# Optimization experiments

Hardware: AMD Instinct MI355X
Metric: run time of the kernel (lower is better)

The kernel has to match this reference:

```python
import jax, jax.numpy as jnp
import numpy as np

K = 3  # dynamic kernel size


def _conv(x, w, b, pad):
    # x: [B,Cin,H,W], w: [Cout,Cin,kh,kw]
    y = jax.lax.conv_general_dilated(
        x, w, window_strides=(1, 1), padding=pad,
        dimension_numbers=("NCHW", "OIHW", "NCHW"))
    return y + b[None, :, None, None]


def setup_inputs() -> dict:
    key = jax.random.key(0)
    ks = jax.random.split(key, 9)
    B, C, H, W = 16, 256, 64, 64
    sc1 = 1.0 / np.sqrt(C * 9)
    sc3 = 1.0 / np.sqrt(C)
    return {
        "x":    jax.random.normal(ks[0], (B, C, H, W), jnp.float32),
        "kin":  jax.random.normal(ks[1], (B, C, H, W), jnp.float32),
        "w1":   jax.random.normal(ks[2], (C, C, 3, 3), jnp.float32) * sc1,
        "b1":   jax.random.normal(ks[3], (C,), jnp.float32) * 0.01,
        "w2":   jax.random.normal(ks[4], (C, C, 3, 3), jnp.float32) * sc1,
        "b2":   jax.random.normal(ks[5], (C,), jnp.float32) * 0.01,
        "w3":   jax.random.normal(ks[6], (K * K * C, C, 1, 1), jnp.float32) * sc3,
        "b3":   jax.random.normal(ks[7], (K * K * C,), jnp.float32) * 0.01,
        "bias": jax.random.normal(ks[8], (C,), jnp.float32) * 0.01,
    }


def reference(x, kin, w1, b1, w2, b2, w3, b3, bias):
    B, C, H, W = x.shape
    # tokernel: conv3x3 (valid) -> lrelu(0.1) -> conv3x3 -> lrelu -> global avg pool -> 1x1 conv
    h = jax.nn.leaky_relu(_conv(kin, w1, b1, "VALID"), 0.1)
    h = jax.nn.leaky_relu(_conv(h, w2, b2, "VALID"), 0.1)
    p = h.mean(axis=(2, 3))                                   # [B,C] adaptive avg pool 1x1
    kern = jnp.einsum("bc,oc->bo", p, w3.reshape(K * K * C, C)) + b3  # 1x1 conv
    kern = kern.reshape(B, C, 1, K, K)                        # per-sample depthwise weights

    pad = [(K // 2, K // 2)] * 2

    def dw(xi, wi):  # xi: [C,H,W], wi: [C,1,K,K]
        return jax.lax.conv_general_dilated(
            xi[None], wi, window_strides=(1, 1), padding=pad,
            dimension_numbers=("NCHW", "OIHW", "NCHW"),
            feature_group_count=C)[0]

    y = jax.vmap(dw)(x, kern)                                 # [B,C,H,W]
    return y + bias[None, :, None, None]
```

## Files before the change

kernel.cpp:

```cpp
#include <hip/hip_runtime.h>
#include <hip/hip_bf16.h>
#include <stdint.h>

#define CCH 256

typedef __attribute__((ext_vector_type(8))) short short8;
typedef __attribute__((ext_vector_type(4))) float f32x4;

__device__ __forceinline__ float lrelu(float v) { return v > 0.f ? v : 0.1f * v; }

__device__ __forceinline__ unsigned short f2bf(float f) {
    __hip_bfloat16 h = __float2bfloat16(f);
    return *reinterpret_cast<unsigned short*>(&h);
}

__device__ __forceinline__ void gl_lds16(const void* g, void* s) {
    __builtin_amdgcn_global_load_lds(
        (const __attribute__((address_space(1))) unsigned int*)(uintptr_t)g,
        (__attribute__((address_space(3))) unsigned int*)(unsigned int)(uintptr_t)s,
        16, 0, 0);
}

__device__ __forceinline__ void pipe_barrier() {
    asm volatile("" ::: "memory");
    __builtin_amdgcn_s_barrier();
    asm volatile("" ::: "memory");
}

__global__ __launch_bounds__(256)
void nhwc_k(const float* __restrict__ in, unsigned short* __restrict__ out)
{
    __shared__ float t[32][65];
    const int tid = threadIdx.x;
    const int kc = blockIdx.x, y = blockIdx.y, b = blockIdx.z;
    const float* src = in + ((size_t)(b * 256 + kc * 32)) * 4096 + y * 64;
#pragma unroll
    for (int i = 0; i < 2; ++i) {
        int idx = tid + i * 256;
        int cl = idx >> 4, xg = idx & 15;
        float4 v = *(const float4*)(src + (size_t)cl * 4096 + xg * 4);
        t[cl][xg * 4 + 0] = v.x; t[cl][xg * 4 + 1] = v.y;
        t[cl][xg * 4 + 2] = v.z; t[cl][xg * 4 + 3] = v.w;
    }
    __syncthreads();
    const int x = tid >> 2, cg = tid & 3;
    union { unsigned short us[8]; uint4 v; } u;
#pragma unroll
    for (int j = 0; j < 8; ++j) u.us[j] = f2bf(t[cg * 8 + j][x]);
    unsigned short* dst = out + (((size_t)(b * 8 + kc) * 4096 + y * 64 + x) * 32 + cg * 8);
    *(uint4*)dst = u.v;
}

__global__ __launch_bounds__(256)
void wtr_k(const float* __restrict__ w1, const float* __restrict__ w2,
           unsigned short* __restrict__ o1, unsigned short* __restrict__ o2)
{
    const int ss = blockIdx.x;
    const int kc = ss / 9, t = ss - kc * 9;
    const float* w = blockIdx.y ? w2 : w1;
    unsigned short* o = blockIdx.y ? o2 : o1;
#pragma unroll
    for (int rep = 0; rep < 4; ++rep) {
        int slot = threadIdx.x + rep * 256;
        int f = slot >> 6, l = slot & 63;
        int co = f * 16 + (l & 15);
        int q  = l >> 4;
        union { unsigned short us[8]; uint4 v; } u;
#pragma unroll
        for (int uu = 0; uu < 8; ++uu)
            u.us[uu] = f2bf(w[((size_t)co * 256 + kc * 32 + q * 8 + uu) * 9 + t]);
        *(uint4*)(o + (size_t)ss * 8192 + slot * 8) = u.v;
    }
}

__global__ __launch_bounds__(256)
void zero_pool_k(float* __restrict__ p) { p[blockIdx.x * 256 + threadIdx.x] = 0.f; }

template<int POOL, int WIN, int WOUT>
__global__ __launch_bounds__(256, 2)
void convmm_k(const unsigned short* __restrict__ im, const unsigned short* __restrict__ wt,
              const float* __restrict__ bias, unsigned short* __restrict__ outp,
              float* __restrict__ pool)
{
    constexpr int HINPIX = WIN * WIN;
    constexpr int NVAL   = WOUT * WOUT;
    constexpr int NB = 16 * 512 + 8 * 512;
    __shared__ __align__(16) short Ls[3 * NB];

    const int tid  = threadIdx.x;
    const int wave = tid >> 6;
    const int lane = tid & 63;
    const int quad = lane >> 4;
    const int l15  = lane & 15;
    const int wm   = (wave & 1) * 128;
    const int wn   = (wave >> 1) * 64;
    const int nb0  = blockIdx.x * 128;
    const int b    = blockIdx.y;

    const unsigned short* abase = wt + (size_t)(wave * 4) * 512 + (size_t)lane * 8;
    size_t bofs[2];
#pragma unroll
    for (int h = 0; h < 2; ++h) {
        int nn = nb0 + (wave * 2 + h) * 16 + l15;
        if (nn > NVAL - 1) nn = NVAL - 1;
        int y = nn / WOUT, x = nn - y * WOUT;
        bofs[h] = ((size_t)(b * 8) * HINPIX + (size_t)y * WIN + x) * 32 + quad * 8;
    }

    f32x4 acc[8][4];
#pragma unroll
    for (int i = 0; i < 8; ++i)
#pragma unroll
        for (int j = 0; j < 4; ++j) { f32x4 z = {0.f, 0.f, 0.f, 0.f}; acc[i][j] = z; }

    auto stage = [&](int ss, short* buf) {
        const int kc = ss / 9, t = ss - kc * 9;
        const int ky = t / 3, kx = t - ky * 3;
        const size_t aoff = (size_t)ss * 8192;
        const size_t boff = ((size_t)kc * HINPIX + (size_t)ky * WIN + kx) * 32;
        short* bl = buf + 16 * 512;
#pragma unroll
        for (int h = 0; h < 4; ++h)
            gl_lds16(abase + aoff + h * 512, buf + (wave * 4 + h) * 512);
#pragma unroll
        for (int h = 0; h < 2; ++h)
            gl_lds16(im + bofs[h] + boff, bl + (wave * 2 + h) * 512);
    };

    auto compute = [&](const short* buf) {
        const short* ap = buf + (size_t)(wave & 1) * 8 * 512 + lane * 8;
        const short* bp = buf + 16 * 512 + (size_t)(wave >> 1) * 4 * 512 + lane * 8;
        short8 a[8], bfr[4];
#pragma unroll
        for (int i = 0; i < 8; ++i)
            a[i]  = *(const short8*)(ap + i * 512);
#pragma unroll
        for (int j = 0; j < 4; ++j)
            bfr[j] = *(const short8*)(bp + j * 512);
        __builtin_amdgcn_s_setprio(1);
#pragma unroll
        for (int i = 0; i < 8; ++i)
#pragma unroll
            for (int j = 0; j < 4; ++j)
                acc[i][j] = __builtin_amdgcn_mfma_f32_16x16x32_bf16(a[i], bfr[j], acc[i][j], 0, 0, 0);
        __builtin_amdgcn_s_setprio(0);
    };

    short* B0 = Ls;
    short* B1 = Ls + NB;
    short* B2 = Ls + 2 * NB;

    stage(0, B0);
    stage(1, B1);
    asm volatile("s_waitcnt vmcnt(6)" ::: "memory");
    pipe_barrier();

    short *c0 = B0, *c1 = B1, *c2 = B2;
    for (int s = 0; s < 70; ++s) {
        stage(s + 2, c2);
        compute(c0);
        asm volatile("s_waitcnt vmcnt(6)" ::: "memory");
        pipe_barrier();
        short* t = c0; c0 = c1; c1 = c2; c2 = t;
    }
    compute(c0);
    asm volatile("s_waitcnt vmcnt(0)" ::: "memory");
    pipe_barrier();
    compute(c1);

    const int co_l = wm + quad * 4;
    if (!POOL) {
#pragma unroll
        for (int i = 0; i < 8; ++i) {
            const int c0i = co_l + i * 16;
            float4 bv = *(const float4*)(bias + c0i);
            unsigned short* dstp = outp + ((size_t)(b * 8 + (c0i >> 5)) * NVAL) * 32 + (c0i & 31);
#pragma unroll
            for (int j = 0; j < 4; ++j) {
                int nn = nb0 + wn + j * 16 + l15;
                if (nn < NVAL) {
                    ushort4 pk = make_ushort4(
                        f2bf(lrelu(acc[i][j].x + bv.x)),
                        f2bf(lrelu(acc[i][j].y + bv.y)),
                        f2bf(lrelu(acc[i][j].z + bv.z)),
                        f2bf(lrelu(acc[i][j].w + bv.w)));
                    *(ushort4*)(dstp + (size_t)nn * 32) = pk;
                }
            }
        }
    } else {
#pragma unroll
        for (int i = 0; i < 8; ++i) {
            const int c0i = co_l + i * 16;
            float4 bv = *(const float4*)(bias + c0i);
            float s0 = 0.f, s1 = 0.f, s2 = 0.f, s3 = 0.f;
#pragma unroll
            for (int j = 0; j < 4; ++j) {
                int nn = nb0 + wn + j * 16 + l15;
                if (nn < NVAL) {
                    s0 += lrelu(acc[i][j].x + bv.x);
                    s1 += lrelu(acc[i][j].y + bv.y);
                    s2 += lrelu(acc[i][j].z + bv.z);
                    s3 += lrelu(acc[i][j].w + bv.w);
                }
            }
#pragma unroll
            for (int off = 1; off < 16; off <<= 1) {
                s0 += __shfl_xor(s0, off, 64);
                s1 += __shfl_xor(s1, off, 64);
                s2 += __shfl_xor(s2, off, 64);
                s3 += __shfl_xor(s3, off, 64);
            }
            if (l15 == 0) {
                float* pp = pool + b * 256 + c0i;
                atomicAdd(pp + 0, s0); atomicAdd(pp + 1, s1);
                atomicAdd(pp + 2, s2); atomicAdd(pp + 3, s3);
            }
        }
    }
}

__global__ __launch_bounds__(256)
void kern_gemm_k(const float* __restrict__ p, const float* __restrict__ w3,
                 const float* __restrict__ b3, float* __restrict__ kern)
{
    const int b = blockIdx.y;
    const int o = blockIdx.x * 256 + threadIdx.x;
    __shared__ float pv[CCH];
    pv[threadIdx.x] = p[b * CCH + threadIdx.x] * (1.f / 3600.f);
    __syncthreads();
    float acc = b3[o];
    const float* wr = w3 + (size_t)o * CCH;
#pragma unroll 4
    for (int c = 0; c < CCH; c += 4) {
        float4 wv = *(const float4*)(wr + c);
        acc += wv.x * pv[c] + wv.y * pv[c + 1] + wv.z * pv[c + 2] + wv.w * pv[c + 3];
    }
    kern[(size_t)b * (9 * CCH) + o] = acc;
}

__global__ __launch_bounds__(256)
void dw_k(const float* __restrict__ x, const float* __restrict__ kern,
          const float* __restrict__ bias, float* __restrict__ out)
{
    __shared__ float t[66 * 67];
    const int tid = threadIdx.x;
    const int bc = blockIdx.x;
    const int c = bc & (CCH - 1);
    const int b = bc >> 8;

#pragma unroll
    for (int i = 0; i < 18; ++i) {
        int idx = tid + i * 256;
        if (idx < 66 * 67) t[idx] = 0.f;
    }

    const float* kp = kern + (size_t)b * (9 * CCH) + c * 9;
    float k[9];
#pragma unroll
    for (int q = 0; q < 9; ++q) k[q] = kp[q];
    const float bs = bias[c];
    const float* xp = x + (size_t)bc * 4096;
    float* op = out + (size_t)bc * 4096;
    __syncthreads();

#pragma unroll
    for (int i = 0; i < 4; ++i) {
        int p4 = tid + i * 256;
        float4 v = *(const float4*)(xp + p4 * 4);
        int yy = p4 >> 4, xx = (p4 & 15) * 4;
        float* d = &t[(yy + 1) * 67 + 1 + xx];
        d[0] = v.x; d[1] = v.y; d[2] = v.z; d[3] = v.w;
    }
    __syncthreads();

#pragma unroll
    for (int i = 0; i < 4; ++i) {
        int p4 = tid + i * 256;
        int yy = p4 >> 4, xx = (p4 & 15) * 4;
        float r[3][6];
#pragma unroll
        for (int dy = 0; dy < 3; ++dy)
#pragma unroll
            for (int dx = 0; dx < 6; ++dx)
                r[dy][dx] = t[(yy + dy) * 67 + xx + dx];
        float4 o;
        float* ov = (float*)&o;
#pragma unroll
        for (int j = 0; j < 4; ++j) {
            float a = bs;
#pragma unroll
            for (int dy = 0; dy < 3; ++dy)
#pragma unroll
                for (int dx = 0; dx < 3; ++dx)
                    a += k[dy * 3 + dx] * r[dy][j + dx];
            ov[j] = a;
        }
        *(float4*)(op + p4 * 4) = o;
    }
}

extern "C" void kernel_launch(void* const* d_in, const int* in_sizes, int n_in,
                              void* d_out, int out_size, void* d_ws, size_t ws_size,
                              hipStream_t stream)
{
    const float* x    = (const float*)d_in[0];
    const float* kin  = (const float*)d_in[1];
    const float* w1   = (const float*)d_in[2];
    const float* b1   = (const float*)d_in[3];
    const float* w2   = (const float*)d_in[4];
    const float* b2   = (const float*)d_in[5];
    const float* w3   = (const float*)d_in[6];
    const float* b3   = (const float*)d_in[7];
    const float* bias = (const float*)d_in[8];

    unsigned short* imA = (unsigned short*)d_ws;
    unsigned short* h1  = imA + (size_t)16 * 8 * 4096 * 32;
    unsigned short* w1t = h1 + (size_t)16 * 8 * 3844 * 32 + 8192;
    unsigned short* w2t = w1t + (size_t)72 * 8192;
    float* pool = (float*)(w2t + (size_t)72 * 8192);
    float* kern = pool + 16 * 256;

    float* out = (float*)d_out;

    hipLaunchKernelGGL(zero_pool_k, dim3(16), dim3(256), 0, stream, pool);
    hipLaunchKernelGGL(nhwc_k, dim3(8, 64, 16), dim3(256), 0, stream, kin, imA);
    hipLaunchKernelGGL(wtr_k, dim3(72, 2), dim3(256), 0, stream, w1, w2, w1t, w2t);
    hipLaunchKernelGGL((convmm_k<0, 64, 62>), dim3(31, 16), dim3(256), 0, stream,
                       imA, w1t, b1, h1, (float*)nullptr);
    hipLaunchKernelGGL((convmm_k<1, 62, 60>), dim3(29, 16), dim3(256), 0, stream,
                       h1, w2t, b2, (unsigned short*)nullptr, pool);
    hipLaunchKernelGGL(kern_gemm_k, dim3(9, 16), dim3(256), 0, stream, pool, w3, b3, kern);
    hipLaunchKernelGGL(dw_k, dim3(16 * 256), dim3(256), 0, stream, x, kern, bias, out);
}
```

Baseline: 332.6 us.

## Fuse prep kernels, fold kernel GEMM into depthwise, load conv B operand directly to registers

Merges the NHWC transpose, weight transpose and pool zeroing into one launch. It also removes the separate kernel-weight GEMM by having each depthwise block compute its own 9 taps from the pooled vector with wave reductions. Inside the conv GEMM, the activation (B) operand is now loaded straight into registers with a two-deep register pipeline instead of being staged through LDS, which shrinks LDS use. Together these cut launch overhead and LDS traffic, at the cost of redundant w3 reads per depthwise block and more register pressure in the GEMM.

After: 349.1 us. 1.05x slower.

```diff
diff --git a/kernel.cpp b/kernel.cpp
--- a/kernel.cpp
+++ b/kernel.cpp
@@ -28,10 +28,37 @@
 }
 
 __global__ __launch_bounds__(256)
-void nhwc_k(const float* __restrict__ in, unsigned short* __restrict__ out)
+void pre_k(const float* __restrict__ in, unsigned short* __restrict__ out,
+           const float* __restrict__ w1, const float* __restrict__ w2,
+           unsigned short* __restrict__ o1, unsigned short* __restrict__ o2,
+           float* __restrict__ pool)
 {
     __shared__ float t[32][65];
     const int tid = threadIdx.x;
+    if (blockIdx.z == 16) {
+        const int flat = blockIdx.x + 8 * blockIdx.y;
+        if (flat < 144) {
+            const int which = flat / 72, ss = flat - which * 72;
+            const int kc = ss / 9, tt = ss - kc * 9;
+            const float* w = which ? w2 : w1;
+            unsigned short* o = which ? o2 : o1;
+#pragma unroll
+            for (int rep = 0; rep < 4; ++rep) {
+                int slot = tid + rep * 256;
+                int f = slot >> 6, l = slot & 63;
+                int co = f * 16 + (l & 15);
+                int q  = l >> 4;
+                union { unsigned short us[8]; uint4 v; } u;
+#pragma unroll
+                for (int uu = 0; uu < 8; ++uu)
+                    u.us[uu] = f2bf(w[((size_t)co * 256 + kc * 32 + q * 8 + uu) * 9 + tt]);
+                *(uint4*)(o + (size_t)ss * 8192 + slot * 8) = u.v;
+            }
+        } else if (flat < 160) {
+            pool[(flat - 144) * 256 + tid] = 0.f;
+        }
+        return;
+    }
     const int kc = blockIdx.x, y = blockIdx.y, b = blockIdx.z;
     const float* src = in + ((size_t)(b * 256 + kc * 32)) * 4096 + y * 64;
 #pragma unroll
@@ -50,31 +77,6 @@
     unsigned short* dst = out + (((size_t)(b * 8 + kc) * 4096 + y * 64 + x) * 32 + cg * 8);
     *(uint4*)dst = u.v;
 }
-
-__global__ __launch_bounds__(256)
-void wtr_k(const float* __restrict__ w1, const float* __restrict__ w2,
-           unsigned short* __restrict__ o1, unsigned short* __restrict__ o2)
-{
-    const int ss = blockIdx.x;
-    const int kc = ss / 9, t = ss - kc * 9;
-    const float* w = blockIdx.y ? w2 : w1;
-    unsigned short* o = blockIdx.y ? o2 : o1;
-#pragma unroll
-    for (int rep = 0; rep < 4; ++rep) {
-        int slot = threadIdx.x + rep * 256;
-        int f = slot >> 6, l = slot & 63;
-        int co = f * 16 + (l & 15);
-        int q  = l >> 4;
-        union { unsigned short us[8]; uint4 v; } u;
-#pragma unroll
-        for (int uu = 0; uu < 8; ++uu)
-            u.us[uu] = f2bf(w[((size_t)co * 256 + kc * 32 + q * 8 + uu) * 9 + t]);
-        *(uint4*)(o + (size_t)ss * 8192 + slot * 8) = u.v;
-    }
-}
-
-__global__ __launch_bounds__(256)
-void zero_pool_k(float* __restrict__ p) { p[blockIdx.x * 256 + threadIdx.x] = 0.f; }
 
 template<int POOL, int WIN, int WOUT>
 __global__ __launch_bounds__(256, 2)
@@ -84,7 +86,7 @@
 {
     constexpr int HINPIX = WIN * WIN;
     constexpr int NVAL   = WOUT * WOUT;
-    constexpr int NB = 16 * 512 + 8 * 512;
+    constexpr int NB = 16 * 512;
     __shared__ __align__(16) short Ls[3 * NB];
 
     const int tid  = threadIdx.x;
@@ -98,13 +100,13 @@
     const int b    = blockIdx.y;
 
     const unsigned short* abase = wt + (size_t)(wave * 4) * 512 + (size_t)lane * 8;
-    size_t bofs[2];
-#pragma unroll
-    for (int h = 0; h < 2; ++h) {
-        int nn = nb0 + (wave * 2 + h) * 16 + l15;
+    size_t bofsR[4];
+#pragma unroll
+    for (int j = 0; j < 4; ++j) {
+        int nn = nb0 + wn + j * 16 + l15;
         if (nn > NVAL - 1) nn = NVAL - 1;
         int y = nn / WOUT, x = nn - y * WOUT;
-        bofs[h] = ((size_t)(b * 8) * HINPIX + (size_t)y * WIN + x) * 32 + quad * 8;
+        bofsR[j] = ((size_t)(b * 8) * HINPIX + (size_t)y * WIN + x) * 32 + quad * 8;
     }
 
     f32x4 acc[8][4];
@@ -113,60 +115,67 @@
 #pragma unroll
         for (int j = 0; j < 4; ++j) { f32x4 z = {0.f, 0.f, 0.f, 0.f}; acc[i][j] = z; }
 
-    auto stage = [&](int ss, short* buf) {
+    auto stageA = [&](int ss, short* buf) {
+        const size_t aoff = (size_t)ss * 8192;
+#pragma unroll
+        for (int h = 0; h < 4; ++h)
+            gl_lds16(abase + aoff + h * 512, buf + (wave * 4 + h) * 512);
+    };
+
+    auto loadB = [&](int ss, short8 (&rb)[4]) {
         const int kc = ss / 9, t = ss - kc * 9;
         const int ky = t / 3, kx = t - ky * 3;
-        const size_t aoff = (size_t)ss * 8192;
         const size_t boff = ((size_t)kc * HINPIX + (size_t)ky * WIN + kx) * 32;
-        short* bl = buf + 16 * 512;
-#pragma unroll
-        for (int h = 0; h < 4; ++h)
-            gl_lds16(abase + aoff + h * 512, buf + (wave * 4 + h) * 512);
-#pragma unroll
-        for (int h = 0; h < 2; ++h)
-            gl_lds16(im + bofs[h] + boff, bl + (wave * 2 + h) * 512);
+#pragma unroll
+        for (int j = 0; j < 4; ++j)
+            rb[j] = *(const short8*)(im + bofsR[j] + boff);
     };
 
-    auto compute = [&](const short* buf) {
+    auto compute = [&](const short* buf, const short8 (&rb)[4]) {
         const short* ap = buf + (size_t)(wave & 1) * 8 * 512 + lane * 8;
-        const short* bp = buf + 16 * 512 + (size_t)(wave >> 1) * 4 * 512 + lane * 8;
-        short8 a[8], bfr[4];
+        short8 a[8];
 #pragma unroll
         for (int i = 0; i < 8; ++i)
-            a[i]  = *(const short8*)(ap + i * 512);
-#pragma unroll
-        for (int j = 0; j < 4; ++j)
-            bfr[j] = *(const short8*)(bp + j * 512);
+            a[i] = *(const short8*)(ap + i * 512);
         __builtin_amdgcn_s_setprio(1);
 #pragma unroll
         for (int i = 0; i < 8; ++i)
 #pragma unroll
             for (int j = 0; j < 4; ++j)
-                acc[i][j] = __builtin_amdgcn_mfma_f32_16x16x32_bf16(a[i], bfr[j], acc[i][j], 0, 0, 0);
+                acc[i][j] = __builtin_amdgcn_mfma_f32_16x16x32_bf16(a[i], rb[j], acc[i][j], 0, 0, 0);
         __builtin_amdgcn_s_setprio(0);
     };
 
-    short* B0 = Ls;
-    short* B1 = Ls + NB;
-    short* B2 = Ls + 2 * NB;
-
-    stage(0, B0);
-    stage(1, B1);
-    asm volatile("s_waitcnt vmcnt(6)" ::: "memory");
+    short* c0 = Ls;
+    short* c1 = Ls + NB;
+    short* c2 = Ls + 2 * NB;
+    short8 rb0[4], rb1[4];
+
+    loadB(0, rb0);
+    stageA(0, c0);
+    stageA(1, c1);
+    loadB(1, rb1);
+    asm volatile("s_waitcnt vmcnt(8)" ::: "memory");
     pipe_barrier();
 
-    short *c0 = B0, *c1 = B1, *c2 = B2;
-    for (int s = 0; s < 70; ++s) {
-        stage(s + 2, c2);
-        compute(c0);
-        asm volatile("s_waitcnt vmcnt(6)" ::: "memory");
+    for (int s = 0; s < 70; s += 2) {
+        stageA(s + 2, c2);
+        compute(c0, rb0);
+        loadB(s + 2, rb0);
+        asm volatile("s_waitcnt vmcnt(8)" ::: "memory");
         pipe_barrier();
-        short* t = c0; c0 = c1; c1 = c2; c2 = t;
-    }
-    compute(c0);
+        { short* t = c0; c0 = c1; c1 = c2; c2 = t; }
+        stageA(s + 3, c2);
+        compute(c0, rb1);
+        loadB(s + 3, rb1);
+        asm volatile("s_waitcnt vmcnt(8)" ::: "memory");
+        pipe_barrier();
+        { short* t = c0; c0 = c1; c1 = c2; c2 = t; }
+    }
+    compute(c0, rb0);
     asm volatile("s_waitcnt vmcnt(0)" ::: "memory");
     pipe_barrier();
-    compute(c1);
+    compute(c1, rb1);
 
     const int co_l = wm + quad * 4;
     if (!POOL) {
@@ -221,26 +230,8 @@
 }
 
 __global__ __launch_bounds__(256)
-void kern_gemm_k(const float* __restrict__ p, const float* __restrict__ w3,
-                 const float* __restrict__ b3, float* __restrict__ kern)
-{
-    const int b = blockIdx.y;
-    const int o = blockIdx.x * 256 + threadIdx.x;
-    __shared__ float pv[CCH];
-    pv[threadIdx.x] = p[b * CCH + threadIdx.x] * (1.f / 3600.f);
-    __syncthreads();
-    float acc = b3[o];
-    const float* wr = w3 + (size_t)o * CCH;
-#pragma unroll 4
-    for (int c = 0; c < CCH; c += 4) {
-        float4 wv = *(const float4*)(wr + c);
-        acc += wv.x * pv[c] + wv.y * pv[c + 1] + wv.z * pv[c + 2] + wv.w * pv[c + 3];
-    }
-    kern[(size_t)b * (9 * CCH) + o] = acc;
-}
-
-__global__ __launch_bounds__(256)
-void dw_k(const float* __restrict__ x, const float* __restrict__ kern,
+void dw_k(const float* __restrict__ x, const float* __restrict__ pool,
+          const float* __restrict__ w3, const float* __restrict__ b3,
           const float* __restrict__ bias, float* __restrict__ out)
 {
     __shared__ float t[66 * 67];
@@ -248,17 +239,34 @@
     const int bc = blockIdx.x;
     const int c = bc & (CCH - 1);
     const int b = bc >> 8;
-
-#pragma unroll
-    for (int i = 0; i < 18; ++i) {
-        int idx = tid + i * 256;
-        if (idx < 66 * 67) t[idx] = 0.f;
-    }
-
-    const float* kp = kern + (size_t)b * (9 * CCH) + c * 9;
+    const int lane = tid & 63, wv = tid >> 6;
+
+    const float p = pool[b * CCH + tid] * (1.f / 3600.f);
+    const float* w3r = w3 + (size_t)(c * 9) * CCH + tid;
+    float part[9];
+#pragma unroll
+    for (int q = 0; q < 9; ++q) part[q] = w3r[(size_t)q * CCH] * p;
+#pragma unroll
+    for (int off = 32; off; off >>= 1)
+#pragma unroll
+        for (int q = 0; q < 9; ++q) part[q] += __shfl_down(part[q], off, 64);
+    if (lane == 0) {
+#pragma unroll
+        for (int q = 0; q < 9; ++q) t[wv * 9 + q] = part[q];
+    }
+    __syncthreads();
     float k[9];
 #pragma unroll
-    for (int q = 0; q < 9; ++q) k[q] = kp[q];
+    for (int q = 0; q < 9; ++q)
+        k[q] = t[q] + t[9 + q] + t[18 + q] + t[27 + q] + b3[c * 9 + q];
+    __syncthreads();
+
+    if (tid < 67) { t[tid] = 0.f; t[65 * 67 + tid] = 0.f; }
+    if (tid >= 128 && tid < 192) {
+        int r = tid - 127;
+        t[r * 67] = 0.f; t[r * 67 + 65] = 0.f;
+    }
+
     const float bs = bias[c];
     const float* xp = x + (size_t)bc * 4096;
     float* op = out + (size_t)bc * 4096;
@@ -319,17 +327,15 @@
     unsigned short* w1t = h1 + (size_t)16 * 8 * 3844 * 32 + 8192;
     unsigned short* w2t = w1t + (size_t)72 * 8192;
     float* pool = (float*)(w2t + (size_t)72 * 8192);
-    float* kern = pool + 16 * 256;
 
     float* out = (float*)d_out;
 
-    hipLaunchKernelGGL(zero_pool_k, dim3(16), dim3(256), 0, stream, pool);
-    hipLaunchKernelGGL(nhwc_k, dim3(8, 64, 16), dim3(256), 0, stream, kin, imA);
-    hipLaunchKernelGGL(wtr_k, dim3(72, 2), dim3(256), 0, stream, w1, w2, w1t, w2t);
+    hipLaunchKernelGGL(pre_k, dim3(8, 64, 17), dim3(256), 0, stream,
+                       kin, imA, w1, w2, w1t, w2t, pool);
     hipLaunchKernelGGL((convmm_k<0, 64, 62>), dim3(31, 16), dim3(256), 0, stream,
                        imA, w1t, b1, h1, (float*)nullptr);
     hipLaunchKernelGGL((convmm_k<1, 62, 60>), dim3(29, 16), dim3(256), 0, stream,
                        h1, w2t, b2, (unsigned short*)nullptr, pool);
-    hipLaunchKernelGGL(kern_gemm_k, dim3(9, 16), dim3(256), 0, stream, pool, w3, b3, kern);
-    hipLaunchKernelGGL(dw_k, dim3(16 * 256), dim3(256), 0, stream, x, kern, bias, out);
-}
+    hipLaunchKernelGGL(dw_k, dim3(16 * 256), dim3(256), 0, stream,
+                       x, pool, w3, b3, bias, out);
+}
```
